# Kernel optimization log

Hardware: AMD Instinct MI355X
Metric: run time of the kernel (lower is better)

Reference implementation:

```python
import jax, jax.numpy as jnp
import numpy as np
import math

B, T, IN_DIM = 4, 1024, 64
D, H, L, DFF = 1024, 16, 4, 4096
N_STEPS = 24
MAXLEN = 2048
DK = D // H


def _pos_encoding(max_len, d):
    pos = np.arange(max_len, dtype=np.float32)[:, None]
    div = np.exp(np.arange(0, d, 2, dtype=np.float32) * (-math.log(10000.0) / d))
    pe = np.zeros((max_len, d), dtype=np.float32)
    pe[:, 0::2] = np.sin(pos * div)
    pe[:, 1::2] = np.cos(pos * div)
    return jnp.asarray(pe)

_PE = _pos_encoding(MAXLEN, D)


def _lin(x, W, b):
    # torch Linear convention: W is (out, in)
    return x @ W.T + b


def _mha(q, kv, Wq, bq, Wk, bk, Wv, bv, Wo, bo):
    Bq, Tq, _ = q.shape
    Tk = kv.shape[1]
    Qh = _lin(q, Wq, bq).reshape(Bq, Tq, H, DK).transpose(0, 2, 1, 3)
    Kh = _lin(kv, Wk, bk).reshape(Bq, Tk, H, DK).transpose(0, 2, 1, 3)
    Vh = _lin(kv, Wv, bv).reshape(Bq, Tk, H, DK).transpose(0, 2, 1, 3)
    scores = jnp.einsum('bhqd,bhkd->bhqk', Qh, Kh) / math.sqrt(DK)
    probs = jax.nn.softmax(scores, axis=-1)
    out = jnp.einsum('bhqk,bhkd->bhqd', probs, Vh)
    out = out.transpose(0, 2, 1, 3).reshape(Bq, Tq, D)
    return _lin(out, Wo, bo)


def _ffn(x, W1, b1, W2, b2):
    return _lin(jax.nn.relu(_lin(x, W1, b1)), W2, b2)


def _ln(x, g, b, eps=1e-5):
    mu = jnp.mean(x, axis=-1, keepdims=True)
    var = jnp.var(x, axis=-1, keepdims=True)
    return (x - mu) / jnp.sqrt(var + eps) * g + b


def setup_inputs() -> dict:
    key = jax.random.key(0)
    ks = iter(jax.random.split(key, 64))
    def w(shape, s=0.02):
        return jax.random.normal(next(ks), shape, jnp.float32) * s
    inp = {'x': jax.random.normal(next(ks), (B, T, IN_DIM), jnp.float32)}
    inp['in_W'] = w((D, IN_DIM)); inp['in_b'] = jnp.zeros((D,), jnp.float32)
    for p in ['enc', 'dec']:
        for n in ['Wq', 'Wk', 'Wv', 'Wo']:
            inp[f'{p}_{n}'] = w((L, D, D))
            inp[f'{p}_b{n[1].lower()}'] = jnp.zeros((L, D), jnp.float32)
    for p in ['ffe', 'ffd']:
        inp[f'{p}_W1'] = w((DFF, D)); inp[f'{p}_b1'] = jnp.zeros((DFF,), jnp.float32)
        inp[f'{p}_W2'] = w((D, DFF)); inp[f'{p}_b2'] = jnp.zeros((D,), jnp.float32)
    for p in ['ne', 'nd']:
        inp[f'{p}_g'] = jnp.ones((D,), jnp.float32); inp[f'{p}_b'] = jnp.zeros((D,), jnp.float32)
    inp['out_W'] = w((1, D)); inp['out_b'] = jnp.zeros((1,), jnp.float32)
    inp['temb_W'] = w((D, 1)); inp['temb_b'] = jnp.zeros((D,), jnp.float32)
    return inp


def reference(x, in_W, in_b,
              enc_Wq, enc_bq, enc_Wk, enc_bk, enc_Wv, enc_bv, enc_Wo, enc_bo,
              ffe_W1, ffe_b1, ffe_W2, ffe_b2, ne_g, ne_b,
              dec_Wq, dec_bq, dec_Wk, dec_bk, dec_Wv, dec_bv, dec_Wo, dec_bo,
              ffd_W1, ffd_b1, ffd_W2, ffd_b2, nd_g, nd_b,
              out_W, out_b, temb_W, temb_b):
    batch, seq, _ = x.shape
    h = _lin(x, in_W, in_b) + _PE[:seq]
    for l in range(L):
        h = _mha(h, h, enc_Wq[l], enc_bq[l], enc_Wk[l], enc_bk[l],
                 enc_Wv[l], enc_bv[l], enc_Wo[l], enc_bo[l])
        h = _ln(h + _ffn(h, ffe_W1, ffe_b1, ffe_W2, ffe_b2), ne_g, ne_b)
    dec = jnp.zeros((batch, 1, D), x.dtype)
    preds = []
    for _ in range(N_STEPS):
        d = dec + _PE[:dec.shape[1]]
        for l in range(L):
            # same layer weights used for self- and cross-attention, as in source
            d = _mha(d, d, dec_Wq[l], dec_bq[l], dec_Wk[l], dec_bk[l],
                     dec_Wv[l], dec_bv[l], dec_Wo[l], dec_bo[l])
            d = _mha(d, h, dec_Wq[l], dec_bq[l], dec_Wk[l], dec_bk[l],
                     dec_Wv[l], dec_bv[l], dec_Wo[l], dec_bo[l])
            d = _ln(d + _ffn(d, ffd_W1, ffd_b1, ffd_W2, ffd_b2), nd_g, nd_b)
        step = _lin(d[:, -1, :], out_W, out_b)        # (B, 1)
        preds.append(step[:, None, :])                 # (B, 1, 1)
        emb = _lin(step, temb_W, temb_b)[:, None, :]   # (B, 1, D)
        dec = jnp.concatenate([dec, emb], axis=1)
    return jnp.concatenate(preds, axis=1)              # (B, n_steps, 1)
```

## Files before the change

kernel.cpp:

```cpp
#include <hip/hip_runtime.h>
#include <math.h>

#define DM    1024
#define NH    16
#define DKH   64
#define NL    4
#define DFFN  4096
#define BB    4
#define TT    1024
#define NSTEP 24
#define BT    (BB*TT)
#define MD    (BB*NSTEP)
#define CSPLIT 8
#define CKEYS  (TT/CSPLIT)

typedef __attribute__((ext_vector_type(8))) short s16x8;
typedef __attribute__((ext_vector_type(4))) short s16x4;
typedef __attribute__((ext_vector_type(4))) float f32x4;

__device__ inline short f2b(float f){
  unsigned u = __float_as_uint(f);
  u += 0x7fffu + ((u>>16)&1u);
  return (short)(u>>16);
}
__device__ inline float b2f(short h){
  return __uint_as_float(((unsigned)(unsigned short)h)<<16);
}

__global__ __launch_bounds__(256)
void split_kernel(const float* __restrict__ X, short* __restrict__ Hi,
                  short* __restrict__ Lo, int n8)
{
  const size_t i = (size_t)blockIdx.x*256 + threadIdx.x;
  if (i >= (size_t)n8) return;
  const float4 v0 = *(const float4*)(X + i*8);
  const float4 v1 = *(const float4*)(X + i*8 + 4);
  const float f[8] = {v0.x,v0.y,v0.z,v0.w,v1.x,v1.y,v1.z,v1.w};
  s16x8 hv, lv;
  #pragma unroll
  for (int e=0;e<8;e++){
    const short h = f2b(f[e]);
    hv[e] = h;
    lv[e] = f2b(f[e] - b2f(h));
  }
  *(s16x8*)(Hi + i*8) = hv;
  *(s16x8*)(Lo + i*8) = lv;
}

__global__ void zero_kernel(float* __restrict__ p, int n) {
  int i = blockIdx.x*256 + threadIdx.x;
  if (i < n) p[i] = 0.f;
}

__global__ __launch_bounds__(256)
void add_pe_split(const float* __restrict__ h, short* __restrict__ Hi,
                  short* __restrict__ Lo)
{
  const int row = blockIdx.x;
  const int pos = row & (TT-1);
  const int d = threadIdx.x*4;
  const float4 a = *(const float4*)(h + (size_t)row*DM + d);
  const float c1 = -9.210340371976184f / 1024.0f;
  const float e0 = expf((float)d * c1);
  const float e1 = expf((float)(d+2) * c1);
  const float a0 = (float)pos * e0, a1 = (float)pos * e1;
  const float v[4] = {a.x + sinf(a0), a.y + cosf(a0), a.z + sinf(a1), a.w + cosf(a1)};
  s16x4 hv, lv;
  #pragma unroll
  for (int e=0;e<4;e++){
    const short hb = f2b(v[e]);
    hv[e] = hb;
    lv[e] = f2b(v[e] - b2f(hb));
  }
  *(s16x4*)(Hi + (size_t)row*DM + d) = hv;
  *(s16x4*)(Lo + (size_t)row*DM + d) = lv;
}

__global__ __launch_bounds__(256)
void dec_prep_split(short* __restrict__ Dhi, short* __restrict__ Dlo,
                    const float* __restrict__ tok)
{
  const int r = blockIdx.x;
  const int i = r >> 2;
  const int d = threadIdx.x*4;
  const float4 a = *(const float4*)(tok + (size_t)r*DM + d);
  const float c1 = -9.210340371976184f / 1024.0f;
  const float e0 = expf((float)d * c1);
  const float e1 = expf((float)(d+2) * c1);
  const float a0 = (float)i * e0, a1 = (float)i * e1;
  const float v[4] = {a.x + sinf(a0), a.y + cosf(a0), a.z + sinf(a1), a.w + cosf(a1)};
  s16x4 hv, lv;
  #pragma unroll
  for (int e=0;e<4;e++){
    const short hb = f2b(v[e]);
    hv[e] = hb;
    lv[e] = f2b(v[e] - b2f(hb));
  }
  *(s16x4*)(Dhi + (size_t)r*DM + d) = hv;
  *(s16x4*)(Dlo + (size_t)r*DM + d) = lv;
}

template<int ACT, int OUT_MODE>
__global__ __launch_bounds__(256, 2)
void gemm_split(const short* __restrict__ Ahi, const short* __restrict__ Alo,
                const short* __restrict__ Bhi, const short* __restrict__ Blo,
                const float* __restrict__ bias,
                float* __restrict__ C, short* __restrict__ Chi, short* __restrict__ Clo,
                int M, int N, int K)
{
  __shared__ __align__(16) short lA[2][128][40];
  __shared__ __align__(16) short lB[2][128][40];
  const int tid = threadIdx.x;
  const int m0 = blockIdx.x*128, n0 = blockIdx.y*128;
  const int lane = tid & 63, w = tid >> 6;
  const int wr = w >> 1, wc = w & 1;
  const int fr = lane & 15, fq = lane >> 4;

  f32x4 acc[4][4];
  #pragma unroll
  for (int i=0;i<4;i++)
    #pragma unroll
    for (int j=0;j<4;j++) acc[i][j] = (f32x4){0.f,0.f,0.f,0.f};

  for (int k0 = 0; k0 < K; k0 += 32) {
    __syncthreads();
    #pragma unroll
    for (int j=0;j<2;j++){
      const int cc = tid + j*256;
      const int row = cc >> 2, kq = cc & 3;
      const size_t ga = (size_t)(m0+row)*K + k0 + kq*8;
      const size_t gb = (size_t)(n0+row)*K + k0 + kq*8;
      *(s16x8*)&lA[0][row][kq*8] = *(const s16x8*)(Ahi + ga);
      *(s16x8*)&lA[1][row][kq*8] = *(const s16x8*)(Alo + ga);
      *(s16x8*)&lB[0][row][kq*8] = *(const s16x8*)(Bhi + gb);
      *(s16x8*)&lB[1][row][kq*8] = *(const s16x8*)(Blo + gb);
    }
    __syncthreads();
    s16x8 ah[4], al[4], bh[4], bl[4];
    #pragma unroll
    for (int i=0;i<4;i++){
      ah[i] = *(const s16x8*)&lA[0][wr*64+i*16+fr][fq*8];
      al[i] = *(const s16x8*)&lA[1][wr*64+i*16+fr][fq*8];
    }
    #pragma unroll
    for (int j=0;j<4;j++){
      bh[j] = *(const s16x8*)&lB[0][wc*64+j*16+fr][fq*8];
      bl[j] = *(const s16x8*)&lB[1][wc*64+j*16+fr][fq*8];
    }
    #pragma unroll
    for (int i=0;i<4;i++)
      #pragma unroll
      for (int j=0;j<4;j++){
        acc[i][j] = __builtin_amdgcn_mfma_f32_16x16x32_bf16(ah[i], bh[j], acc[i][j], 0,0,0);
        acc[i][j] = __builtin_amdgcn_mfma_f32_16x16x32_bf16(ah[i], bl[j], acc[i][j], 0,0,0);
        acc[i][j] = __builtin_amdgcn_mfma_f32_16x16x32_bf16(al[i], bh[j], acc[i][j], 0,0,0);
      }
  }
  #pragma unroll
  for (int j=0;j<4;j++){
    const int col = n0 + wc*64 + j*16 + fr;
    const float bv = bias[col];
    #pragma unroll
    for (int i=0;i<4;i++){
      const int row0 = m0 + wr*64 + i*16 + fq*4;
      #pragma unroll
      for (int r=0;r<4;r++){
        float v = acc[i][j][r] + bv;
        if (ACT==1) v = fmaxf(v, 0.f);
        const size_t idx = (size_t)(row0+r)*N + col;
        if (OUT_MODE==0 || OUT_MODE==2) C[idx] = v;
        if (OUT_MODE==1 || OUT_MODE==2){
          const short hb = f2b(v);
          Chi[idx] = hb;
          Clo[idx] = f2b(v - b2f(hb));
        }
        if (OUT_MODE==3) Chi[idx] = f2b(v);
      }
    }
  }
}

template<int MR>
__global__ __launch_bounds__(256)
void gemm_dec(const short* __restrict__ Ahi, const short* __restrict__ Alo,
              const short* __restrict__ B0hi, const short* __restrict__ B0lo,
              const short* __restrict__ B1hi, const short* __restrict__ B1lo,
              const short* __restrict__ B2hi, const short* __restrict__ B2lo,
              float* __restrict__ part, int N, int K, int KS)
{
  const short* Bhi = (blockIdx.z==0) ? B0hi : (blockIdx.z==1 ? B1hi : B2hi);
  const short* Blo = (blockIdx.z==0) ? B0lo : (blockIdx.z==1 ? B1lo : B2lo);
  float* P = part + ((size_t)blockIdx.z*KS + blockIdx.y)*(size_t)MD*N;
  const int KK = K / KS;
  const int kbase = blockIdx.y * KK;
  const int n0 = blockIdx.x * 128;
  __shared__ __align__(16) short lA[2][96][40];
  __shared__ __align__(16) short lB[2][128][40];
  const int tid = threadIdx.x;
  const int lane = tid & 63, w = tid >> 6;
  const int fr = lane & 15, fq = lane >> 4;
  constexpr int CH = MR*128;

  f32x4 acc[MR][2];
  #pragma unroll
  for (int i=0;i<MR;i++){ acc[i][0]=(f32x4){0,0,0,0}; acc[i][1]=(f32x4){0,0,0,0}; }

  for (int k0 = kbase; k0 < kbase + KK; k0 += 32) {
    __syncthreads();
    #pragma unroll
    for (int t=0; t<(CH+255)/256; t++){
      const int cc = tid + t*256;
      if (cc < CH){
        const int row = cc>>3, hl = (cc>>2)&1, kq = cc&3;
        const short* src = hl ? Alo : Ahi;
        *(s16x8*)&lA[hl][row][kq*8] = *(const s16x8*)(src + (size_t)row*K + k0 + kq*8);
      }
    }
    #pragma unroll
    for (int t=0; t<4; t++){
      const int cc = tid + t*256;
      const int row = cc>>3, hl = (cc>>2)&1, kq = cc&3;
      const short* src = hl ? Blo : Bhi;
      *(s16x8*)&lB[hl][row][kq*8] = *(const s16x8*)(src + (size_t)(n0+row)*K + k0 + kq*8);
    }
    __syncthreads();
    s16x8 bh[2], bl[2];
    #pragma unroll
    for (int j=0;j<2;j++){
      bh[j] = *(const s16x8*)&lB[0][w*32+j*16+fr][fq*8];
      bl[j] = *(const s16x8*)&lB[1][w*32+j*16+fr][fq*8];
    }
    #pragma unroll
    for (int i=0;i<MR;i++){
      const s16x8 ah = *(const s16x8*)&lA[0][i*16+fr][fq*8];
      const s16x8 al = *(const s16x8*)&lA[1][i*16+fr][fq*8];
      #pragma unroll
      for (int j=0;j<2;j++){
        acc[i][j] = __builtin_amdgcn_mfma_f32_16x16x32_bf16(ah, bh[j], acc[i][j], 0,0,0);
        acc[i][j] = __builtin_amdgcn_mfma_f32_16x16x32_bf16(ah, bl[j], acc[i][j], 0,0,0);
        acc[i][j] = __builtin_amdgcn_mfma_f32_16x16x32_bf16(al, bh[j], acc[i][j], 0,0,0);
      }
    }
  }
  #pragma unroll
  for (int j=0;j<2;j++){
    const int col = n0 + w*32 + j*16 + fr;
    #pragma unroll
    for (int i=0;i<MR;i++){
      const int row0 = i*16 + fq*4;
      #pragma unroll
      for (int r=0;r<4;r++)
        P[(size_t)(row0+r)*N + col] = acc[i][j][r];
    }
  }
}

template<int ACT, int MODE>
__global__ __launch_bounds__(256)
void reduce_dec(const float* __restrict__ part,
                const float* __restrict__ b0, const float* __restrict__ b1,
                const float* __restrict__ b2,
                float* __restrict__ o0, float* __restrict__ o1, float* __restrict__ o2,
                short* __restrict__ ohi, short* __restrict__ olo,
                int N, int KS)
{
  const int idx = blockIdx.x*256 + threadIdx.x;
  const int z = blockIdx.y;
  const float* P = part + (size_t)z*KS*(size_t)MD*N;
  const float* bias = (z==0)?b0:(z==1?b1:b2);
  float* out = (z==0)?o0:(z==1?o1:o2);
  float s = 0.f;
  for (int ks=0; ks<KS; ks++) s += P[(size_t)ks*MD*N + idx];
  s += bias[idx & (N-1)];
  if (ACT==1) s = fmaxf(s, 0.f);
  if (MODE==0 || MODE==2) out[idx] = s;
  if (MODE==1 || MODE==2){
    if (z==0){
      const short hb = f2b(s);
      ohi[idx] = hb;
      olo[idx] = f2b(s - b2f(hb));
    }
  }
}

__global__ __launch_bounds__(256)
void attn_enc(const float* __restrict__ Qg, const float* __restrict__ Kg,
              const float* __restrict__ Vg, short* __restrict__ Ohi,
              short* __restrict__ Olo)
{
  const int bh = blockIdx.y;
  const int b = bh >> 4, hh = bh & 15;
  const int row = blockIdx.x*256 + threadIdx.x;
  const size_t base = ((size_t)b*TT)*DM + hh*DKH;
  float q[64];
  {
    const float* qp = Qg + base + (size_t)row*DM;
    #pragma unroll
    for (int d4=0; d4<16; d4++){
      const float4 v = *(const float4*)(qp + d4*4);
      q[d4*4+0]=v.x; q[d4*4+1]=v.y; q[d4*4+2]=v.z; q[d4*4+3]=v.w;
    }
  }
  float o[64];
  #pragma unroll
  for (int d=0;d<64;d++) o[d]=0.f;
  float m = -INFINITY, l = 0.f;
  __shared__ float Ks[64][68];
  __shared__ float Vs[64][68];
  for (int kt=0; kt<TT; kt+=64) {
    __syncthreads();
    #pragma unroll
    for (int t=0;t<4;t++){
      const int fi = threadIdx.x + t*256;
      const int j = fi>>4, dq = fi&15;
      *(float4*)&Ks[j][dq*4] = *(const float4*)(Kg + base + (size_t)(kt+j)*DM + dq*4);
      *(float4*)&Vs[j][dq*4] = *(const float4*)(Vg + base + (size_t)(kt+j)*DM + dq*4);
    }
    __syncthreads();
    for (int j=0;j<64;j++){
      float s0=0.f,s1=0.f,s2=0.f,s3=0.f;
      #pragma unroll
      for (int d=0; d<64; d+=4){
        s0 = fmaf(q[d+0], Ks[j][d+0], s0);
        s1 = fmaf(q[d+1], Ks[j][d+1], s1);
        s2 = fmaf(q[d+2], Ks[j][d+2], s2);
        s3 = fmaf(q[d+3], Ks[j][d+3], s3);
      }
      const float s = ((s0+s1)+(s2+s3)) * 0.125f;
      if (s > m) {
        const float f = __expf(m - s);
        l *= f;
        #pragma unroll
        for (int d=0;d<64;d++) o[d] *= f;
        m = s;
      }
      const float p = __expf(s - m);
      l += p;
      #pragma unroll
      for (int d=0;d<64;d++) o[d] = fmaf(p, Vs[j][d], o[d]);
    }
  }
  const float inv = 1.f / l;
  #pragma unroll
  for (int d8=0; d8<8; d8++){
    s16x8 hv, lv;
    #pragma unroll
    for (int e=0;e<8;e++){
      const float f = o[d8*8+e]*inv;
      const short hb = f2b(f);
      hv[e] = hb;
      lv[e] = f2b(f - b2f(hb));
    }
    *(s16x8*)(Ohi + base + (size_t)row*DM + d8*8) = hv;
    *(s16x8*)(Olo + base + (size_t)row*DM + d8*8) = lv;
  }
}

__global__ __launch_bounds__(256)
void attn_dec_selfp(const float* __restrict__ Qg, const float* __restrict__ Kg,
                    const float* __restrict__ Vg, short* __restrict__ Ohi,
                    short* __restrict__ Olo, int n)
{
  const int b = blockIdx.x >> 4, hh = blockIdx.x & 15;
  const size_t base = (size_t)b*DM + hh*DKH;
  __shared__ float Qs[NSTEP][68], Ks[NSTEP][68], Vs[NSTEP][68];
  __shared__ float P[NSTEP][28];
  const int tid = threadIdx.x;
  for (int t = tid; t < 3*n*16; t += 256) {
    const int tensor = t / (n*16);
    const int fi = t - tensor*(n*16);
    const int row = fi >> 4, dq = fi & 15;
    const float* src = (tensor==0?Qg:(tensor==1?Kg:Vg)) + base + (size_t)(row*4)*DM + dq*4;
    float (*dst)[68] = (tensor==0?Qs:(tensor==1?Ks:Vs));
    *(float4*)&dst[row][dq*4] = *(const float4*)src;
  }
  __syncthreads();
  for (int idx = tid; idx < n*n; idx += 256) {
    const int i = idx / n, j = idx - i*n;
    float s0=0.f,s1=0.f,s2=0.f,s3=0.f;
    #pragma unroll
    for (int d=0; d<64; d+=4){
      s0 = fmaf(Qs[i][d+0], Ks[j][d+0], s0);
      s1 = fmaf(Qs[i][d+1], Ks[j][d+1], s1);
      s2 = fmaf(Qs[i][d+2], Ks[j][d+2], s2);
      s3 = fmaf(Qs[i][d+3], Ks[j][d+3], s3);
    }
    P[i][j] = ((s0+s1)+(s2+s3))*0.125f;
  }
  __syncthreads();
  if (tid < n) {
    float mm = -INFINITY;
    for (int j=0;j<n;j++) mm = fmaxf(mm, P[tid][j]);
    float l = 0.f;
    for (int j=0;j<n;j++){ const float p = __expf(P[tid][j]-mm); P[tid][j]=p; l+=p; }
    const float inv = 1.f/l;
    for (int j=0;j<n;j++) P[tid][j] *= inv;
  }
  __syncthreads();
  for (int idx = tid; idx < n*64; idx += 256){
    const int i = idx >> 6, d = idx & 63;
    float s = 0.f;
    for (int j=0;j<n;j++) s = fmaf(P[i][j], Vs[j][d], s);
    const short hb = f2b(s);
    const size_t o = base + (size_t)(i*4)*DM + d;
    Ohi[o] = hb;
    Olo[o] = f2b(s - b2f(hb));
  }
}

__global__ __launch_bounds__(256)
void attn_cross_part(const float* __restrict__ Qg, const short* __restrict__ Kc,
                     const short* __restrict__ Vc, float* __restrict__ opart,
                     float* __restrict__ mlpart, int n)
{
  const int ks = blockIdx.x;
  const int bh = blockIdx.y;
  const int b = bh >> 4, hh = bh & 15;
  __shared__ float Qs[NSTEP][68];
  __shared__ float KVs[CKEYS][68];
  __shared__ float S[NSTEP][CKEYS+4];
  const int tid = threadIdx.x;
  const size_t qbase = (size_t)b*DM + hh*DKH;
  for (int t=tid; t<n*16; t+=256){
    const int row = t>>4, dq = t&15;
    *(float4*)&Qs[row][dq*4] = *(const float4*)(Qg + qbase + (size_t)(row*4)*DM + dq*4);
  }
  const size_t kbase = ((size_t)b*TT + (size_t)ks*CKEYS)*DM + hh*DKH;
  for (int t=tid; t<CKEYS*8; t+=256){
    const int row = t>>3, d8 = t&7;
    const s16x8 v = *(const s16x8*)(Kc + kbase + (size_t)row*DM + d8*8);
    #pragma unroll
    for (int e=0;e<8;e++) KVs[row][d8*8+e] = b2f(v[e]);
  }
  __syncthreads();
  for (int idx=tid; idx<n*128; idx+=256){
    const int i = idx >> 7, j = idx & 127;
    float s0=0.f,s1=0.f,s2=0.f,s3=0.f;
    #pragma unroll
    for (int d=0; d<64; d+=4){
      s0 = fmaf(Qs[i][d+0], KVs[j][d+0], s0);
      s1 = fmaf(Qs[i][d+1], KVs[j][d+1], s1);
      s2 = fmaf(Qs[i][d+2], KVs[j][d+2], s2);
      s3 = fmaf(Qs[i][d+3], KVs[j][d+3], s3);
    }
    S[i][j] = ((s0+s1)+(s2+s3))*0.125f;
  }
  __syncthreads();
  for (int t=tid; t<CKEYS*8; t+=256){
    const int row = t>>3, d8 = t&7;
    const s16x8 v = *(const s16x8*)(Vc + kbase + (size_t)row*DM + d8*8);
    #pragma unroll
    for (int e=0;e<8;e++) KVs[row][d8*8+e] = b2f(v[e]);
  }
  if (tid < n){
    float mm=-INFINITY;
    for (int j=0;j<CKEYS;j++) mm = fmaxf(mm, S[tid][j]);
    float l=0.f;
    for (int j=0;j<CKEYS;j++){ const float p=__expf(S[tid][j]-mm); S[tid][j]=p; l+=p; }
    mlpart[((size_t)bh*CSPLIT+ks)*(2*NSTEP) + tid*2+0] = mm;
    mlpart[((size_t)bh*CSPLIT+ks)*(2*NSTEP) + tid*2+1] = l;
  }
  __syncthreads();
  for (int idx=tid; idx<n*64; idx+=256){
    const int i = idx >> 6, d = idx & 63;
    float s=0.f;
    for (int j=0;j<CKEYS;j++) s = fmaf(S[i][j], KVs[j][d], s);
    opart[(((size_t)bh*CSPLIT+ks)*NSTEP + i)*DKH + d] = s;
  }
}

__global__ __launch_bounds__(256)
void attn_cross_comb(const float* __restrict__ opart, const float* __restrict__ mlpart,
                     short* __restrict__ Ohi, short* __restrict__ Olo, int n)
{
  const int bh = blockIdx.x;
  const int idx = blockIdx.y*256 + threadIdx.x;
  const int i = idx >> 6, d = idx & 63;
  if (i >= n) return;
  float M = -INFINITY;
  #pragma unroll
  for (int s=0;s<CSPLIT;s++)
    M = fmaxf(M, mlpart[((size_t)bh*CSPLIT+s)*(2*NSTEP) + i*2]);
  float acc = 0.f, L = 0.f;
  #pragma unroll
  for (int s=0;s<CSPLIT;s++){
    const float mm = mlpart[((size_t)bh*CSPLIT+s)*(2*NSTEP) + i*2+0];
    const float ll = mlpart[((size_t)bh*CSPLIT+s)*(2*NSTEP) + i*2+1];
    const float f = __expf(mm - M);
    acc = fmaf(f, opart[(((size_t)bh*CSPLIT+s)*NSTEP + i)*DKH + d], acc);
    L   = fmaf(f, ll, L);
  }
  const int b = bh >> 4, hh = bh & 15;
  const float v = acc / L;
  const short hb = f2b(v);
  const size_t o = ((size_t)(i*4+b))*DM + hh*DKH + d;
  Ohi[o] = hb;
  Olo[o] = f2b(v - b2f(hb));
}

__device__ inline float wave_sum(float v){
  #pragma unroll
  for (int off=1; off<64; off<<=1) v += __shfl_xor(v, off, 64);
  return v;
}

__global__ __launch_bounds__(256)
void ln_add_split(const float* __restrict__ X, const float* __restrict__ Y,
                  const float* __restrict__ g, const float* __restrict__ be,
                  short* __restrict__ Ohi, short* __restrict__ Olo)
{
  const size_t row = blockIdx.x;
  const int tid = threadIdx.x;
  const float4 a = *(const float4*)(X + row*DM + tid*4);
  const float4 b = *(const float4*)(Y + row*DM + tid*4);
  const float v0=a.x+b.x, v1=a.y+b.y, v2=a.z+b.z, v3=a.w+b.w;
  float s = v0+v1+v2+v3;
  float q = v0*v0+v1*v1+v2*v2+v3*v3;
  s = wave_sum(s); q = wave_sum(q);
  __shared__ float rs[4], rq[4];
  if ((tid&63)==0){ rs[tid>>6]=s; rq[tid>>6]=q; }
  __syncthreads();
  const float S = rs[0]+rs[1]+rs[2]+rs[3];
  const float Q = rq[0]+rq[1]+rq[2]+rq[3];
  const float mean = S * (1.f/DM);
  const float var  = Q * (1.f/DM) - mean*mean;
  const float rstd = rsqrtf(var + 1e-5f);
  const float4 gv = *(const float4*)(g  + tid*4);
  const float4 bv = *(const float4*)(be + tid*4);
  const float v[4] = {(v0-mean)*rstd*gv.x + bv.x, (v1-mean)*rstd*gv.y + bv.y,
                      (v2-mean)*rstd*gv.z + bv.z, (v3-mean)*rstd*gv.w + bv.w};
  s16x4 hv, lv;
  #pragma unroll
  for (int e=0;e<4;e++){
    const short hb = f2b(v[e]);
    hv[e] = hb;
    lv[e] = f2b(v[e] - b2f(hb));
  }
  *(s16x4*)(Ohi + row*DM + tid*4) = hv;
  *(s16x4*)(Olo + row*DM + tid*4) = lv;
}

__global__ __launch_bounds__(256)
void ln_add_dec(const float* __restrict__ X, const float* __restrict__ Y,
                const float* __restrict__ g, const float* __restrict__ be,
                float* __restrict__ Outf, short* __restrict__ Ohi,
                short* __restrict__ Olo)
{
  const size_t row = blockIdx.x;
  const int tid = threadIdx.x;
  const float4 a = *(const float4*)(X + row*DM + tid*4);
  const float4 b = *(const float4*)(Y + row*DM + tid*4);
  const float v0=a.x+b.x, v1=a.y+b.y, v2=a.z+b.z, v3=a.w+b.w;
  float s = v0+v1+v2+v3;
  float q = v0*v0+v1*v1+v2*v2+v3*v3;
  s = wave_sum(s); q = wave_sum(q);
  __shared__ float rs[4], rq[4];
  if ((tid&63)==0){ rs[tid>>6]=s; rq[tid>>6]=q; }
  __syncthreads();
  const float S = rs[0]+rs[1]+rs[2]+rs[3];
  const float Q = rq[0]+rq[1]+rq[2]+rq[3];
  const float mean = S * (1.f/DM);
  const float var  = Q * (1.f/DM) - mean*mean;
  const float rstd = rsqrtf(var + 1e-5f);
  const float4 gv = *(const float4*)(g  + tid*4);
  const float4 bv = *(const float4*)(be + tid*4);
  const float v[4] = {(v0-mean)*rstd*gv.x + bv.x, (v1-mean)*rstd*gv.y + bv.y,
                      (v2-mean)*rstd*gv.z + bv.z, (v3-mean)*rstd*gv.w + bv.w};
  float4 of; of.x=v[0]; of.y=v[1]; of.z=v[2]; of.w=v[3];
  *(float4*)(Outf + row*DM + tid*4) = of;
  s16x4 hv, lv;
  #pragma unroll
  for (int e=0;e<4;e++){
    const short hb = f2b(v[e]);
    hv[e] = hb;
    lv[e] = f2b(v[e] - b2f(hb));
  }
  *(s16x4*)(Ohi + row*DM + tid*4) = hv;
  *(s16x4*)(Olo + row*DM + tid*4) = lv;
}

__global__ __launch_bounds__(256)
void out_step(const float* __restrict__ Dv, const float* __restrict__ outW,
              const float* __restrict__ outB, const float* __restrict__ tembW,
              const float* __restrict__ tembB, float* __restrict__ dout,
              float* __restrict__ tok, int s)
{
  const int b = blockIdx.x;
  const int tid = threadIdx.x;
  const float* drow = Dv + ((size_t)(s*4 + b))*DM;
  const float4 dv = *(const float4*)(drow + tid*4);
  const float4 wv = *(const float4*)(outW + tid*4);
  float part = dv.x*wv.x + dv.y*wv.y + dv.z*wv.z + dv.w*wv.w;
  part = wave_sum(part);
  __shared__ float red[4];
  __shared__ float stepv;
  if ((tid&63)==0) red[tid>>6] = part;
  __syncthreads();
  if (tid==0) stepv = red[0]+red[1]+red[2]+red[3] + outB[0];
  __syncthreads();
  const float sv = stepv;
  if (tid==0) dout[b*NSTEP + s] = sv;
  if (s+1 < NSTEP) {
    const int d = tid*4;
    const float4 tw = *(const float4*)(tembW + d);
    const float4 tb = *(const float4*)(tembB + d);
    float4 e;
    e.x = fmaf(sv, tw.x, tb.x); e.y = fmaf(sv, tw.y, tb.y);
    e.z = fmaf(sv, tw.z, tb.z); e.w = fmaf(sv, tw.w, tb.w);
    *(float4*)(tok + ((size_t)((s+1)*4 + b))*DM + d) = e;
  }
}

extern "C" void kernel_launch(void* const* d_in, const int* in_sizes, int n_in,
                              void* d_out, int out_size, void* d_ws, size_t ws_size,
                              hipStream_t stream)
{
  (void)in_sizes; (void)n_in; (void)out_size; (void)ws_size;
  const float* x      = (const float*)d_in[0];
  const float* in_W   = (const float*)d_in[1];
  const float* in_b   = (const float*)d_in[2];
  const float* enc_Wq = (const float*)d_in[3];
  const float* enc_bq = (const float*)d_in[4];
  const float* enc_Wk = (const float*)d_in[5];
  const float* enc_bk = (const float*)d_in[6];
  const float* enc_Wv = (const float*)d_in[7];
  const float* enc_bv = (const float*)d_in[8];
  const float* enc_Wo = (const float*)d_in[9];
  const float* enc_bo = (const float*)d_in[10];
  const float* dec_Wq = (const float*)d_in[11];
  const float* dec_bq = (const float*)d_in[12];
  const float* dec_Wk = (const float*)d_in[13];
  const float* dec_bk = (const float*)d_in[14];
  const float* dec_Wv = (const float*)d_in[15];
  const float* dec_bv = (const float*)d_in[16];
  const float* dec_Wo = (const float*)d_in[17];
  const float* dec_bo = (const float*)d_in[18];
  const float* ffe_W1 = (const float*)d_in[19];
  const float* ffe_b1 = (const float*)d_in[20];
  const float* ffe_W2 = (const float*)d_in[21];
  const float* ffe_b2 = (const float*)d_in[22];
  const float* ffd_W1 = (const float*)d_in[23];
  const float* ffd_b1 = (const float*)d_in[24];
  const float* ffd_W2 = (const float*)d_in[25];
  const float* ffd_b2 = (const float*)d_in[26];
  const float* ne_g   = (const float*)d_in[27];
  const float* ne_b   = (const float*)d_in[28];
  const float* nd_g   = (const float*)d_in[29];
  const float* nd_b   = (const float*)d_in[30];
  const float* out_W  = (const float*)d_in[31];
  const float* out_b  = (const float*)d_in[32];
  const float* temb_W = (const float*)d_in[33];
  const float* temb_b = (const float*)d_in[34];
  float* dout = (float*)d_out;

  float* ws = (float*)d_ws;
  size_t off = 0;
  auto alloc  = [&](size_t n){ n = (n+3)&~(size_t)3; float* p = ws + off; off += n; return p; };
  auto allocS = [&](size_t n){ size_t nf = ((n+1)/2 + 3)&~(size_t)3; short* p = (short*)(ws + off); off += nf; return p; };

  short* hshi = allocS((size_t)BT*DM);
  short* hslo = allocS((size_t)BT*DM);
  float* h    = alloc((size_t)BT*DM);
  float* hn   = h;
  float* t0   = alloc((size_t)BT*DM);
  float* t1   = alloc((size_t)BT*DM);
  float* t2   = alloc((size_t)BT*DM);
  short* t3hi = allocS((size_t)BT*DM);
  short* t3lo = allocS((size_t)BT*DM);
  short* hnhi = allocS((size_t)BT*DM);
  short* hnlo = allocS((size_t)BT*DM);
  float* t4   = alloc((size_t)BT*DM);
  float* part = t4;
  short* fmhi = (short*)t0;
  short* fmlo = fmhi + (size_t)BT*DFFN;
  short* kcb  = allocS((size_t)NL*BT*DM);
  short* vcb  = allocS((size_t)NL*BT*DM);
  short* xshi = allocS((size_t)BT*64);
  short* xslo = allocS((size_t)BT*64);
  short* iwhi = allocS((size_t)DM*64);
  short* iwlo = allocS((size_t)DM*64);
  short* w0hi = allocS((size_t)DM*DM); short* w0lo = allocS((size_t)DM*DM);
  short* w1hi = allocS((size_t)DM*DM); short* w1lo = allocS((size_t)DM*DM);
  short* w2hi = allocS((size_t)DM*DM); short* w2lo = allocS((size_t)DM*DM);
  short* w3hi = allocS((size_t)DM*DM); short* w3lo = allocS((size_t)DM*DM);
  short* wfhi = allocS((size_t)DFFN*DM); short* wflo = allocS((size_t)DFFN*DM);
  float* tok  = alloc((size_t)MD*DM);
  float* dbuf = alloc((size_t)MD*DM);
  float* dq   = alloc((size_t)MD*DM);
  float* dk   = alloc((size_t)MD*DM);
  float* dv_  = alloc((size_t)MD*DM);
  float* dffo = alloc((size_t)MD*DM);
  short* dbhi = allocS((size_t)MD*DM);  short* dblo = allocS((size_t)MD*DM);
  short* dahi = allocS((size_t)MD*DM);  short* dalo = allocS((size_t)MD*DM);
  short* dmhi = allocS((size_t)MD*DFFN);short* dmlo = allocS((size_t)MD*DFFN);
  float* opart= alloc((size_t)BB*NH*CSPLIT*NSTEP*DKH);
  float* mlp  = alloc((size_t)BB*NH*CSPLIT*2*NSTEP);

  const size_t MM = (size_t)DM*DM;
  short* dwq = (short*)t0;
  short* dwk = (short*)t1;
  short* dwv = (short*)t2;
  short* dwo = (short*)h;
  short* fw1h = t3hi; short* fw1l = t3lo;
  short* fw2h = hnhi; short* fw2l = hnlo;

  auto cvt = [&](const float* src, short* hi, short* lo, size_t n){
    split_kernel<<<(int)((n/8 + 255)/256), 256, 0, stream>>>(src, hi, lo, (int)(n/8));
  };

  cvt(x,    xshi, xslo, (size_t)BT*64);
  cvt(in_W, iwhi, iwlo, (size_t)DM*64);
  zero_kernel<<<(MD*DM+255)/256, 256, 0, stream>>>(tok, MD*DM);

  gemm_split<0,0><<<dim3(BT/128, DM/128), 256, 0, stream>>>(
      xshi, xslo, iwhi, iwlo, in_b, h, (short*)nullptr, (short*)nullptr, BT, DM, 64);
  add_pe_split<<<BT, 256, 0, stream>>>(h, hshi, hslo);

  for (int l=0; l<NL; ++l) {
    const size_t wo = (size_t)l*DM*DM, bo_ = (size_t)l*DM;
    cvt(enc_Wq+wo, w0hi, w0lo, MM);
    cvt(enc_Wk+wo, w1hi, w1lo, MM);
    cvt(enc_Wv+wo, w2hi, w2lo, MM);
    cvt(enc_Wo+wo, w3hi, w3lo, MM);
    gemm_split<0,0><<<dim3(32,8),256,0,stream>>>(hshi, hslo, w0hi, w0lo, enc_bq+bo_,
        t0, (short*)nullptr, (short*)nullptr, BT, DM, DM);
    gemm_split<0,0><<<dim3(32,8),256,0,stream>>>(hshi, hslo, w1hi, w1lo, enc_bk+bo_,
        t1, (short*)nullptr, (short*)nullptr, BT, DM, DM);
    gemm_split<0,0><<<dim3(32,8),256,0,stream>>>(hshi, hslo, w2hi, w2lo, enc_bv+bo_,
        t2, (short*)nullptr, (short*)nullptr, BT, DM, DM);
    attn_enc<<<dim3(TT/256, BB*NH),256,0,stream>>>(t0, t1, t2, t3hi, t3lo);
    gemm_split<0,2><<<dim3(32,8),256,0,stream>>>(t3hi, t3lo, w3hi, w3lo, enc_bo+bo_,
        hn, hnhi, hnlo, BT, DM, DM);
    cvt(ffe_W1, wfhi, wflo, (size_t)DFFN*DM);
    gemm_split<1,1><<<dim3(32,32),256,0,stream>>>(hnhi, hnlo, wfhi, wflo, ffe_b1,
        (float*)nullptr, fmhi, fmlo, BT, DFFN, DM);
    cvt(ffe_W2, wfhi, wflo, (size_t)DM*DFFN);
    gemm_split<0,0><<<dim3(32,8),256,0,stream>>>(fmhi, fmlo, wfhi, wflo, ffe_b2,
        t4, (short*)nullptr, (short*)nullptr, BT, DM, DFFN);
    ln_add_split<<<BT,256,0,stream>>>(hn, t4, ne_g, ne_b, hshi, hslo);
  }

  for (int l=0; l<NL; ++l) {
    const size_t wo = (size_t)l*DM*DM, bo_ = (size_t)l*DM;
    cvt(dec_Wk+wo, w0hi, w0lo, MM);
    cvt(dec_Wv+wo, w1hi, w1lo, MM);
    gemm_split<0,3><<<dim3(32,8),256,0,stream>>>(hshi, hslo, w0hi, w0lo, dec_bk+bo_,
        (float*)nullptr, kcb+(size_t)l*BT*DM, (short*)nullptr, BT, DM, DM);
    gemm_split<0,3><<<dim3(32,8),256,0,stream>>>(hshi, hslo, w1hi, w1lo, dec_bv+bo_,
        (float*)nullptr, vcb+(size_t)l*BT*DM, (short*)nullptr, BT, DM, DM);
  }

  for (int l=0; l<NL; ++l) {
    const size_t wo = (size_t)l*DM*DM;
    cvt(dec_Wq+wo, dwq + (size_t)l*2*MM, dwq + (size_t)l*2*MM + MM, MM);
    cvt(dec_Wk+wo, dwk + (size_t)l*2*MM, dwk + (size_t)l*2*MM + MM, MM);
    cvt(dec_Wv+wo, dwv + (size_t)l*2*MM, dwv + (size_t)l*2*MM + MM, MM);
    cvt(dec_Wo+wo, dwo + (size_t)l*2*MM, dwo + (size_t)l*2*MM + MM, MM);
  }
  cvt(ffd_W1, fw1h, fw1l, (size_t)DFFN*DM);
  cvt(ffd_W2, fw2h, fw2l, (size_t)DM*DFFN);

  #define GD(MRv, grid, ...) do { switch(MRv){ \
    case 1: gemm_dec<1><<<grid,256,0,stream>>>(__VA_ARGS__); break; \
    case 2: gemm_dec<2><<<grid,256,0,stream>>>(__VA_ARGS__); break; \
    case 3: gemm_dec<3><<<grid,256,0,stream>>>(__VA_ARGS__); break; \
    case 4: gemm_dec<4><<<grid,256,0,stream>>>(__VA_ARGS__); break; \
    case 5: gemm_dec<5><<<grid,256,0,stream>>>(__VA_ARGS__); break; \
    default: gemm_dec<6><<<grid,256,0,stream>>>(__VA_ARGS__); break; } } while(0)

  for (int s=0; s<NSTEP; ++s) {
    const int n = s+1;
    const int rows = 4*n;
    const int Mt = (rows + 15) & ~15;
    const int MR = Mt >> 4;
    dec_prep_split<<<rows,256,0,stream>>>(dbhi, dblo, tok);
    for (int l=0; l<NL; ++l) {
      const size_t bo_ = (size_t)l*DM;
      short* qh = dwq + (size_t)l*2*MM; short* ql = qh + MM;
      short* kh = dwk + (size_t)l*2*MM; short* kl = kh + MM;
      short* vh = dwv + (size_t)l*2*MM; short* vl = vh + MM;
      short* oh = dwo + (size_t)l*2*MM; short* ol = oh + MM;
      GD(MR, dim3(8,8,3), dbhi,dblo, qh,ql, kh,kl, vh,vl, part, DM, DM, 8);
      reduce_dec<0,0><<<dim3(Mt*4,3),256,0,stream>>>(part, dec_bq+bo_, dec_bk+bo_, dec_bv+bo_,
          dq, dk, dv_, (short*)nullptr, (short*)nullptr, DM, 8);
      attn_dec_selfp<<<BB*NH,256,0,stream>>>(dq, dk, dv_, dahi, dalo, n);
      GD(MR, dim3(8,8,1), dahi,dalo, oh,ol, oh,ol, oh,ol, part, DM, DM, 8);
      reduce_dec<0,1><<<dim3(Mt*4,1),256,0,stream>>>(part, dec_bo+bo_, dec_bo+bo_, dec_bo+bo_,
          (float*)nullptr,(float*)nullptr,(float*)nullptr, dbhi, dblo, DM, 8);
      GD(MR, dim3(8,8,1), dbhi,dblo, qh,ql, qh,ql, qh,ql, part, DM, DM, 8);
      reduce_dec<0,0><<<dim3(Mt*4,1),256,0,stream>>>(part, dec_bq+bo_, dec_bq+bo_, dec_bq+bo_,
          dq, dq, dq, (short*)nullptr, (short*)nullptr, DM, 8);
      attn_cross_part<<<dim3(CSPLIT, BB*NH),256,0,stream>>>(dq, kcb+(size_t)l*BT*DM,
          vcb+(size_t)l*BT*DM, opart, mlp, n);
      attn_cross_comb<<<dim3(BB*NH, 6),256,0,stream>>>(opart, mlp, dahi, dalo, n);
      GD(MR, dim3(8,8,1), dahi,dalo, oh,ol, oh,ol, oh,ol, part, DM, DM, 8);
      reduce_dec<0,2><<<dim3(Mt*4,1),256,0,stream>>>(part, dec_bo+bo_, dec_bo+bo_, dec_bo+bo_,
          dbuf, dbuf, dbuf, dbhi, dblo, DM, 8);
      GD(MR, dim3(32,8,1), dbhi,dblo, fw1h,fw1l, fw1h,fw1l, fw1h,fw1l, part, DFFN, DM, 8);
      reduce_dec<1,1><<<dim3(Mt*16,1),256,0,stream>>>(part, ffd_b1, ffd_b1, ffd_b1,
          (float*)nullptr,(float*)nullptr,(float*)nullptr, dmhi, dmlo, DFFN, 8);
      GD(MR, dim3(8,16,1), dmhi,dmlo, fw2h,fw2l, fw2h,fw2l, fw2h,fw2l, part, DM, DFFN, 16);
      reduce_dec<0,0><<<dim3(Mt*4,1),256,0,stream>>>(part, ffd_b2, ffd_b2, ffd_b2,
          dffo, dffo, dffo, (short*)nullptr, (short*)nullptr, DM, 16);
      ln_add_dec<<<rows,256,0,stream>>>(dbuf, dffo, nd_g, nd_b, dbuf, dbhi, dblo);
    }
    out_step<<<BB,256,0,stream>>>(dbuf, out_W, out_b, temb_W, temb_b, dout, tok, s);
  }
  #undef GD
}
```

Measured before the change: 16.50 ms.

## Fold decoder out-projection into next Q projection and fuse decoder reduce kernels

Measured after the change: 13.60 ms. 17.6% less time.

```diff
diff --git a/kernel.cpp b/kernel.cpp
--- a/kernel.cpp
+++ b/kernel.cpp
@@ -13,6 +13,7 @@
 #define MD    (BB*NSTEP)
 #define CSPLIT 8
 #define CKEYS  (TT/CSPLIT)
+#define PSTRIDE ((size_t)MD*DM)
 
 typedef __attribute__((ext_vector_type(8))) short s16x8;
 typedef __attribute__((ext_vector_type(4))) short s16x4;
@@ -25,6 +26,12 @@
 }
 __device__ inline float b2f(short h){
   return __uint_as_float(((unsigned)(unsigned short)h)<<16);
+}
+
+__device__ inline float wave_sum(float v){
+  #pragma unroll
+  for (int off=1; off<64; off<<=1) v += __shfl_xor(v, off, 64);
+  return v;
 }
 
 __global__ __launch_bounds__(256)
@@ -50,6 +57,38 @@
 __global__ void zero_kernel(float* __restrict__ p, int n) {
   int i = blockIdx.x*256 + threadIdx.x;
   if (i < n) p[i] = 0.f;
+}
+
+__global__ __launch_bounds__(256)
+void k_transpose(const float* __restrict__ A, float* __restrict__ At)
+{
+  __shared__ float tile[32][33];
+  const int bx = blockIdx.x & 31, by = blockIdx.x >> 5;
+  const int x0 = bx*32, y0 = by*32;
+  const int tid = threadIdx.x;
+  for (int i=tid; i<1024; i+=256){
+    const int r = i>>5, c = i&31;
+    tile[r][c] = A[(size_t)(y0+r)*DM + x0+c];
+  }
+  __syncthreads();
+  for (int i=tid; i<1024; i+=256){
+    const int r = i>>5, c = i&31;
+    At[(size_t)(x0+r)*DM + y0+c] = tile[c][r];
+  }
+}
+
+__global__ __launch_bounds__(256)
+void k_bc(const float* __restrict__ Wq, const float* __restrict__ bo,
+          const float* __restrict__ bq, float* __restrict__ bc)
+{
+  const int row = blockIdx.x, tid = threadIdx.x;
+  float s = 0.f;
+  for (int j=tid; j<DM; j+=256) s += Wq[(size_t)row*DM + j]*bo[j];
+  s = wave_sum(s);
+  __shared__ float r4[4];
+  if ((tid&63)==0) r4[tid>>6] = s;
+  __syncthreads();
+  if (tid==0) bc[row] = r4[0]+r4[1]+r4[2]+r4[3] + bq[row];
 }
 
 __global__ __launch_bounds__(256)
@@ -74,30 +113,6 @@
   }
   *(s16x4*)(Hi + (size_t)row*DM + d) = hv;
   *(s16x4*)(Lo + (size_t)row*DM + d) = lv;
-}
-
-__global__ __launch_bounds__(256)
-void dec_prep_split(short* __restrict__ Dhi, short* __restrict__ Dlo,
-                    const float* __restrict__ tok)
-{
-  const int r = blockIdx.x;
-  const int i = r >> 2;
-  const int d = threadIdx.x*4;
-  const float4 a = *(const float4*)(tok + (size_t)r*DM + d);
-  const float c1 = -9.210340371976184f / 1024.0f;
-  const float e0 = expf((float)d * c1);
-  const float e1 = expf((float)(d+2) * c1);
-  const float a0 = (float)i * e0, a1 = (float)i * e1;
-  const float v[4] = {a.x + sinf(a0), a.y + cosf(a0), a.z + sinf(a1), a.w + cosf(a1)};
-  s16x4 hv, lv;
-  #pragma unroll
-  for (int e=0;e<4;e++){
-    const short hb = f2b(v[e]);
-    hv[e] = hb;
-    lv[e] = f2b(v[e] - b2f(hb));
-  }
-  *(s16x4*)(Dhi + (size_t)r*DM + d) = hv;
-  *(s16x4*)(Dlo + (size_t)r*DM + d) = lv;
 }
 
 template<int ACT, int OUT_MODE>
@@ -176,109 +191,6 @@
         }
         if (OUT_MODE==3) Chi[idx] = f2b(v);
       }
-    }
-  }
-}
-
-template<int MR>
-__global__ __launch_bounds__(256)
-void gemm_dec(const short* __restrict__ Ahi, const short* __restrict__ Alo,
-              const short* __restrict__ B0hi, const short* __restrict__ B0lo,
-              const short* __restrict__ B1hi, const short* __restrict__ B1lo,
-              const short* __restrict__ B2hi, const short* __restrict__ B2lo,
-              float* __restrict__ part, int N, int K, int KS)
-{
-  const short* Bhi = (blockIdx.z==0) ? B0hi : (blockIdx.z==1 ? B1hi : B2hi);
-  const short* Blo = (blockIdx.z==0) ? B0lo : (blockIdx.z==1 ? B1lo : B2lo);
-  float* P = part + ((size_t)blockIdx.z*KS + blockIdx.y)*(size_t)MD*N;
-  const int KK = K / KS;
-  const int kbase = blockIdx.y * KK;
-  const int n0 = blockIdx.x * 128;
-  __shared__ __align__(16) short lA[2][96][40];
-  __shared__ __align__(16) short lB[2][128][40];
-  const int tid = threadIdx.x;
-  const int lane = tid & 63, w = tid >> 6;
-  const int fr = lane & 15, fq = lane >> 4;
-  constexpr int CH = MR*128;
-
-  f32x4 acc[MR][2];
-  #pragma unroll
-  for (int i=0;i<MR;i++){ acc[i][0]=(f32x4){0,0,0,0}; acc[i][1]=(f32x4){0,0,0,0}; }
-
-  for (int k0 = kbase; k0 < kbase + KK; k0 += 32) {
-    __syncthreads();
-    #pragma unroll
-    for (int t=0; t<(CH+255)/256; t++){
-      const int cc = tid + t*256;
-      if (cc < CH){
-        const int row = cc>>3, hl = (cc>>2)&1, kq = cc&3;
-        const short* src = hl ? Alo : Ahi;
-        *(s16x8*)&lA[hl][row][kq*8] = *(const s16x8*)(src + (size_t)row*K + k0 + kq*8);
-      }
-    }
-    #pragma unroll
-    for (int t=0; t<4; t++){
-      const int cc = tid + t*256;
-      const int row = cc>>3, hl = (cc>>2)&1, kq = cc&3;
-      const short* src = hl ? Blo : Bhi;
-      *(s16x8*)&lB[hl][row][kq*8] = *(const s16x8*)(src + (size_t)(n0+row)*K + k0 + kq*8);
-    }
-    __syncthreads();
-    s16x8 bh[2], bl[2];
-    #pragma unroll
-    for (int j=0;j<2;j++){
-      bh[j] = *(const s16x8*)&lB[0][w*32+j*16+fr][fq*8];
-      bl[j] = *(const s16x8*)&lB[1][w*32+j*16+fr][fq*8];
-    }
-    #pragma unroll
-    for (int i=0;i<MR;i++){
-      const s16x8 ah = *(const s16x8*)&lA[0][i*16+fr][fq*8];
-      const s16x8 al = *(const s16x8*)&lA[1][i*16+fr][fq*8];
-      #pragma unroll
-      for (int j=0;j<2;j++){
-        acc[i][j] = __builtin_amdgcn_mfma_f32_16x16x32_bf16(ah, bh[j], acc[i][j], 0,0,0);
-        acc[i][j] = __builtin_amdgcn_mfma_f32_16x16x32_bf16(ah, bl[j], acc[i][j], 0,0,0);
-        acc[i][j] = __builtin_amdgcn_mfma_f32_16x16x32_bf16(al, bh[j], acc[i][j], 0,0,0);
-      }
-    }
-  }
-  #pragma unroll
-  for (int j=0;j<2;j++){
-    const int col = n0 + w*32 + j*16 + fr;
-    #pragma unroll
-    for (int i=0;i<MR;i++){
-      const int row0 = i*16 + fq*4;
-      #pragma unroll
-      for (int r=0;r<4;r++)
-        P[(size_t)(row0+r)*N + col] = acc[i][j][r];
-    }
-  }
-}
-
-template<int ACT, int MODE>
-__global__ __launch_bounds__(256)
-void reduce_dec(const float* __restrict__ part,
-                const float* __restrict__ b0, const float* __restrict__ b1,
-                const float* __restrict__ b2,
-                float* __restrict__ o0, float* __restrict__ o1, float* __restrict__ o2,
-                short* __restrict__ ohi, short* __restrict__ olo,
-                int N, int KS)
-{
-  const int idx = blockIdx.x*256 + threadIdx.x;
-  const int z = blockIdx.y;
-  const float* P = part + (size_t)z*KS*(size_t)MD*N;
-  const float* bias = (z==0)?b0:(z==1?b1:b2);
-  float* out = (z==0)?o0:(z==1?o1:o2);
-  float s = 0.f;
-  for (int ks=0; ks<KS; ks++) s += P[(size_t)ks*MD*N + idx];
-  s += bias[idx & (N-1)];
-  if (ACT==1) s = fmaxf(s, 0.f);
-  if (MODE==0 || MODE==2) out[idx] = s;
-  if (MODE==1 || MODE==2){
-    if (z==0){
-      const short hb = f2b(s);
-      ohi[idx] = hb;
-      olo[idx] = f2b(s - b2f(hb));
     }
   }
 }
@@ -357,154 +269,6 @@
 }
 
 __global__ __launch_bounds__(256)
-void attn_dec_selfp(const float* __restrict__ Qg, const float* __restrict__ Kg,
-                    const float* __restrict__ Vg, short* __restrict__ Ohi,
-                    short* __restrict__ Olo, int n)
-{
-  const int b = blockIdx.x >> 4, hh = blockIdx.x & 15;
-  const size_t base = (size_t)b*DM + hh*DKH;
-  __shared__ float Qs[NSTEP][68], Ks[NSTEP][68], Vs[NSTEP][68];
-  __shared__ float P[NSTEP][28];
-  const int tid = threadIdx.x;
-  for (int t = tid; t < 3*n*16; t += 256) {
-    const int tensor = t / (n*16);
-    const int fi = t - tensor*(n*16);
-    const int row = fi >> 4, dq = fi & 15;
-    const float* src = (tensor==0?Qg:(tensor==1?Kg:Vg)) + base + (size_t)(row*4)*DM + dq*4;
-    float (*dst)[68] = (tensor==0?Qs:(tensor==1?Ks:Vs));
-    *(float4*)&dst[row][dq*4] = *(const float4*)src;
-  }
-  __syncthreads();
-  for (int idx = tid; idx < n*n; idx += 256) {
-    const int i = idx / n, j = idx - i*n;
-    float s0=0.f,s1=0.f,s2=0.f,s3=0.f;
-    #pragma unroll
-    for (int d=0; d<64; d+=4){
-      s0 = fmaf(Qs[i][d+0], Ks[j][d+0], s0);
-      s1 = fmaf(Qs[i][d+1], Ks[j][d+1], s1);
-      s2 = fmaf(Qs[i][d+2], Ks[j][d+2], s2);
-      s3 = fmaf(Qs[i][d+3], Ks[j][d+3], s3);
-    }
-    P[i][j] = ((s0+s1)+(s2+s3))*0.125f;
-  }
-  __syncthreads();
-  if (tid < n) {
-    float mm = -INFINITY;
-    for (int j=0;j<n;j++) mm = fmaxf(mm, P[tid][j]);
-    float l = 0.f;
-    for (int j=0;j<n;j++){ const float p = __expf(P[tid][j]-mm); P[tid][j]=p; l+=p; }
-    const float inv = 1.f/l;
-    for (int j=0;j<n;j++) P[tid][j] *= inv;
-  }
-  __syncthreads();
-  for (int idx = tid; idx < n*64; idx += 256){
-    const int i = idx >> 6, d = idx & 63;
-    float s = 0.f;
-    for (int j=0;j<n;j++) s = fmaf(P[i][j], Vs[j][d], s);
-    const short hb = f2b(s);
-    const size_t o = base + (size_t)(i*4)*DM + d;
-    Ohi[o] = hb;
-    Olo[o] = f2b(s - b2f(hb));
-  }
-}
-
-__global__ __launch_bounds__(256)
-void attn_cross_part(const float* __restrict__ Qg, const short* __restrict__ Kc,
-                     const short* __restrict__ Vc, float* __restrict__ opart,
-                     float* __restrict__ mlpart, int n)
-{
-  const int ks = blockIdx.x;
-  const int bh = blockIdx.y;
-  const int b = bh >> 4, hh = bh & 15;
-  __shared__ float Qs[NSTEP][68];
-  __shared__ float KVs[CKEYS][68];
-  __shared__ float S[NSTEP][CKEYS+4];
-  const int tid = threadIdx.x;
-  const size_t qbase = (size_t)b*DM + hh*DKH;
-  for (int t=tid; t<n*16; t+=256){
-    const int row = t>>4, dq = t&15;
-    *(float4*)&Qs[row][dq*4] = *(const float4*)(Qg + qbase + (size_t)(row*4)*DM + dq*4);
-  }
-  const size_t kbase = ((size_t)b*TT + (size_t)ks*CKEYS)*DM + hh*DKH;
-  for (int t=tid; t<CKEYS*8; t+=256){
-    const int row = t>>3, d8 = t&7;
-    const s16x8 v = *(const s16x8*)(Kc + kbase + (size_t)row*DM + d8*8);
-    #pragma unroll
-    for (int e=0;e<8;e++) KVs[row][d8*8+e] = b2f(v[e]);
-  }
-  __syncthreads();
-  for (int idx=tid; idx<n*128; idx+=256){
-    const int i = idx >> 7, j = idx & 127;
-    float s0=0.f,s1=0.f,s2=0.f,s3=0.f;
-    #pragma unroll
-    for (int d=0; d<64; d+=4){
-      s0 = fmaf(Qs[i][d+0], KVs[j][d+0], s0);
-      s1 = fmaf(Qs[i][d+1], KVs[j][d+1], s1);
-      s2 = fmaf(Qs[i][d+2], KVs[j][d+2], s2);
-      s3 = fmaf(Qs[i][d+3], KVs[j][d+3], s3);
-    }
-    S[i][j] = ((s0+s1)+(s2+s3))*0.125f;
-  }
-  __syncthreads();
-  for (int t=tid; t<CKEYS*8; t+=256){
-    const int row = t>>3, d8 = t&7;
-    const s16x8 v = *(const s16x8*)(Vc + kbase + (size_t)row*DM + d8*8);
-    #pragma unroll
-    for (int e=0;e<8;e++) KVs[row][d8*8+e] = b2f(v[e]);
-  }
-  if (tid < n){
-    float mm=-INFINITY;
-    for (int j=0;j<CKEYS;j++) mm = fmaxf(mm, S[tid][j]);
-    float l=0.f;
-    for (int j=0;j<CKEYS;j++){ const float p=__expf(S[tid][j]-mm); S[tid][j]=p; l+=p; }
-    mlpart[((size_t)bh*CSPLIT+ks)*(2*NSTEP) + tid*2+0] = mm;
-    mlpart[((size_t)bh*CSPLIT+ks)*(2*NSTEP) + tid*2+1] = l;
-  }
-  __syncthreads();
-  for (int idx=tid; idx<n*64; idx+=256){
-    const int i = idx >> 6, d = idx & 63;
-    float s=0.f;
-    for (int j=0;j<CKEYS;j++) s = fmaf(S[i][j], KVs[j][d], s);
-    opart[(((size_t)bh*CSPLIT+ks)*NSTEP + i)*DKH + d] = s;
-  }
-}
-
-__global__ __launch_bounds__(256)
-void attn_cross_comb(const float* __restrict__ opart, const float* __restrict__ mlpart,
-                     short* __restrict__ Ohi, short* __restrict__ Olo, int n)
-{
-  const int bh = blockIdx.x;
-  const int idx = blockIdx.y*256 + threadIdx.x;
-  const int i = idx >> 6, d = idx & 63;
-  if (i >= n) return;
-  float M = -INFINITY;
-  #pragma unroll
-  for (int s=0;s<CSPLIT;s++)
-    M = fmaxf(M, mlpart[((size_t)bh*CSPLIT+s)*(2*NSTEP) + i*2]);
-  float acc = 0.f, L = 0.f;
-  #pragma unroll
-  for (int s=0;s<CSPLIT;s++){
-    const float mm = mlpart[((size_t)bh*CSPLIT+s)*(2*NSTEP) + i*2+0];
-    const float ll = mlpart[((size_t)bh*CSPLIT+s)*(2*NSTEP) + i*2+1];
-    const float f = __expf(mm - M);
-    acc = fmaf(f, opart[(((size_t)bh*CSPLIT+s)*NSTEP + i)*DKH + d], acc);
-    L   = fmaf(f, ll, L);
-  }
-  const int b = bh >> 4, hh = bh & 15;
-  const float v = acc / L;
-  const short hb = f2b(v);
-  const size_t o = ((size_t)(i*4+b))*DM + hh*DKH + d;
-  Ohi[o] = hb;
-  Olo[o] = f2b(v - b2f(hb));
-}
-
-__device__ inline float wave_sum(float v){
-  #pragma unroll
-  for (int off=1; off<64; off<<=1) v += __shfl_xor(v, off, 64);
-  return v;
-}
-
-__global__ __launch_bounds__(256)
 void ln_add_split(const float* __restrict__ X, const float* __restrict__ Y,
                   const float* __restrict__ g, const float* __restrict__ be,
                   short* __restrict__ Ohi, short* __restrict__ Olo)
@@ -540,21 +304,278 @@
   *(s16x4*)(Olo + row*DM + tid*4) = lv;
 }
 
-__global__ __launch_bounds__(256)
-void ln_add_dec(const float* __restrict__ X, const float* __restrict__ Y,
-                const float* __restrict__ g, const float* __restrict__ be,
-                float* __restrict__ Outf, short* __restrict__ Ohi,
-                short* __restrict__ Olo)
-{
-  const size_t row = blockIdx.x;
+
+template<int MR>
+__global__ __launch_bounds__(256)
+void gemm_dec(const short* __restrict__ Ahi, const short* __restrict__ Alo,
+              const short* __restrict__ B0hi, const short* __restrict__ B0lo,
+              const short* __restrict__ B1hi, const short* __restrict__ B1lo,
+              const short* __restrict__ B2hi, const short* __restrict__ B2lo,
+              float* __restrict__ part, int N, int K, int KS)
+{
+  const short* Bhi = (blockIdx.z==0) ? B0hi : (blockIdx.z==1 ? B1hi : B2hi);
+  const short* Blo = (blockIdx.z==0) ? B0lo : (blockIdx.z==1 ? B1lo : B2lo);
+  float* P = part + ((size_t)blockIdx.z*KS + blockIdx.y)*(size_t)MD*N;
+  const int KK = K / KS;
+  const int kbase = blockIdx.y * KK;
+  const int n0 = blockIdx.x * 128;
+  __shared__ __align__(16) short lA[2][96][40];
+  __shared__ __align__(16) short lB[2][128][40];
   const int tid = threadIdx.x;
-  const float4 a = *(const float4*)(X + row*DM + tid*4);
-  const float4 b = *(const float4*)(Y + row*DM + tid*4);
-  const float v0=a.x+b.x, v1=a.y+b.y, v2=a.z+b.z, v3=a.w+b.w;
+  const int lane = tid & 63, w = tid >> 6;
+  const int fr = lane & 15, fq = lane >> 4;
+  constexpr int CH = MR*128;
+
+  f32x4 acc[MR][2];
+  #pragma unroll
+  for (int i=0;i<MR;i++){ acc[i][0]=(f32x4){0,0,0,0}; acc[i][1]=(f32x4){0,0,0,0}; }
+
+  for (int k0 = kbase; k0 < kbase + KK; k0 += 32) {
+    __syncthreads();
+    #pragma unroll
+    for (int t=0; t<(CH+255)/256; t++){
+      const int cc = tid + t*256;
+      if (cc < CH){
+        const int row = cc>>3, hl = (cc>>2)&1, kq = cc&3;
+        const short* src = hl ? Alo : Ahi;
+        *(s16x8*)&lA[hl][row][kq*8] = *(const s16x8*)(src + (size_t)row*K + k0 + kq*8);
+      }
+    }
+    #pragma unroll
+    for (int t=0; t<4; t++){
+      const int cc = tid + t*256;
+      const int row = cc>>3, hl = (cc>>2)&1, kq = cc&3;
+      const short* src = hl ? Blo : Bhi;
+      *(s16x8*)&lB[hl][row][kq*8] = *(const s16x8*)(src + (size_t)(n0+row)*K + k0 + kq*8);
+    }
+    __syncthreads();
+    s16x8 bh[2], bl[2];
+    #pragma unroll
+    for (int j=0;j<2;j++){
+      bh[j] = *(const s16x8*)&lB[0][w*32+j*16+fr][fq*8];
+      bl[j] = *(const s16x8*)&lB[1][w*32+j*16+fr][fq*8];
+    }
+    #pragma unroll
+    for (int i=0;i<MR;i++){
+      const s16x8 ah = *(const s16x8*)&lA[0][i*16+fr][fq*8];
+      const s16x8 al = *(const s16x8*)&lA[1][i*16+fr][fq*8];
+      #pragma unroll
+      for (int j=0;j<2;j++){
+        acc[i][j] = __builtin_amdgcn_mfma_f32_16x16x32_bf16(ah, bh[j], acc[i][j], 0,0,0);
+        acc[i][j] = __builtin_amdgcn_mfma_f32_16x16x32_bf16(ah, bl[j], acc[i][j], 0,0,0);
+        acc[i][j] = __builtin_amdgcn_mfma_f32_16x16x32_bf16(al, bh[j], acc[i][j], 0,0,0);
+      }
+    }
+  }
+  #pragma unroll
+  for (int j=0;j<2;j++){
+    const int col = n0 + w*32 + j*16 + fr;
+    #pragma unroll
+    for (int i=0;i<MR;i++){
+      const int row0 = i*16 + fq*4;
+      #pragma unroll
+      for (int r=0;r<4;r++)
+        P[(size_t)(row0+r)*N + col] = acc[i][j][r];
+    }
+  }
+}
+
+template<int ACT, int MODE>
+__global__ __launch_bounds__(256)
+void reduce_dec(const float* __restrict__ part,
+                const float* __restrict__ b0, const float* __restrict__ b1,
+                const float* __restrict__ b2,
+                float* __restrict__ o0, float* __restrict__ o1, float* __restrict__ o2,
+                short* __restrict__ ohi, short* __restrict__ olo,
+                int N, int KS)
+{
+  const int idx = blockIdx.x*256 + threadIdx.x;
+  const int z = blockIdx.y;
+  const float* P = part + (size_t)z*KS*(size_t)MD*N;
+  const float* bias = (z==0)?b0:(z==1?b1:b2);
+  float* out = (z==0)?o0:(z==1?o1:o2);
+  float s = 0.f;
+  for (int ks=0; ks<KS; ks++) s += P[(size_t)ks*MD*N + idx];
+  s += bias[idx & (N-1)];
+  if (ACT==1) s = fmaxf(s, 0.f);
+  if (MODE==0 || MODE==2) out[idx] = s;
+  if (MODE==1 || MODE==2){
+    if (z==0){
+      const short hb = f2b(s);
+      ohi[idx] = hb;
+      olo[idx] = f2b(s - b2f(hb));
+    }
+  }
+}
+
+__global__ __launch_bounds__(256)
+void attn_qkv(const float* __restrict__ part,
+              const float* __restrict__ lbq, const float* __restrict__ lbk,
+              const float* __restrict__ lbv,
+              short* __restrict__ Ohi, short* __restrict__ Olo, int n)
+{
+  const int bh = blockIdx.x, b = bh >> 4, hh = bh & 15;
+  const size_t obase = (size_t)b*DM + hh*DKH;
+  __shared__ float Qs[NSTEP][68], Ks[NSTEP][68], Vs[NSTEP][68];
+  __shared__ float P[NSTEP][28];
+  const int tid = threadIdx.x;
+  for (int t = tid; t < 3*n*16; t += 256){
+    const int tensor = t / (n*16);
+    const int fi = t - tensor*(n*16);
+    const int row = fi >> 4, q4 = fi & 15;
+    const int col0 = hh*DKH + q4*4;
+    const float* bias = (tensor==0?lbq:(tensor==1?lbk:lbv));
+    float4 a;
+    a.x = bias[col0]; a.y = bias[col0+1]; a.z = bias[col0+2]; a.w = bias[col0+3];
+    const size_t eoff = (size_t)(row*4+b)*DM + col0;
+    #pragma unroll
+    for (int ks=0; ks<8; ks++){
+      const float4 p = *(const float4*)(part + (size_t)(tensor*8+ks)*PSTRIDE + eoff);
+      a.x+=p.x; a.y+=p.y; a.z+=p.z; a.w+=p.w;
+    }
+    float (*dst)[68] = (tensor==0?Qs:(tensor==1?Ks:Vs));
+    *(float4*)&dst[row][q4*4] = a;
+  }
+  __syncthreads();
+  for (int idx = tid; idx < n*n; idx += 256){
+    const int i = idx / n, j = idx - i*n;
+    float s0=0.f,s1=0.f,s2=0.f,s3=0.f;
+    #pragma unroll
+    for (int d=0; d<64; d+=4){
+      s0 = fmaf(Qs[i][d+0], Ks[j][d+0], s0);
+      s1 = fmaf(Qs[i][d+1], Ks[j][d+1], s1);
+      s2 = fmaf(Qs[i][d+2], Ks[j][d+2], s2);
+      s3 = fmaf(Qs[i][d+3], Ks[j][d+3], s3);
+    }
+    P[i][j] = ((s0+s1)+(s2+s3))*0.125f;
+  }
+  __syncthreads();
+  if (tid < n){
+    float mm = -INFINITY;
+    for (int j=0;j<n;j++) mm = fmaxf(mm, P[tid][j]);
+    float l = 0.f;
+    for (int j=0;j<n;j++){ const float p = __expf(P[tid][j]-mm); P[tid][j]=p; l+=p; }
+    const float inv = 1.f/l;
+    for (int j=0;j<n;j++) P[tid][j] *= inv;
+  }
+  __syncthreads();
+  for (int idx = tid; idx < n*64; idx += 256){
+    const int i = idx >> 6, d = idx & 63;
+    float s = 0.f;
+    for (int j=0;j<n;j++) s = fmaf(P[i][j], Vs[j][d], s);
+    const short hb = f2b(s);
+    const size_t o = obase + (size_t)(i*4)*DM + d;
+    Ohi[o] = hb;
+    Olo[o] = f2b(s - b2f(hb));
+  }
+}
+
+__global__ __launch_bounds__(256)
+void attn_cross_part(const float* __restrict__ Qg, const short* __restrict__ Kc,
+                     const short* __restrict__ Vc, float* __restrict__ opart,
+                     float* __restrict__ mlpart, int n)
+{
+  const int ks = blockIdx.x, bh = blockIdx.y;
+  const int b = bh >> 4, hh = bh & 15;
+  __shared__ float Qs[NSTEP][68];
+  __shared__ short KVs[CKEYS][72];
+  __shared__ float S[NSTEP][132];
+  const int tid = threadIdx.x;
+  const size_t qbase = (size_t)b*DM + hh*DKH;
+  for (int t=tid; t<n*16; t+=256){
+    const int row = t>>4, q4 = t&15;
+    *(float4*)&Qs[row][q4*4] = *(const float4*)(Qg + qbase + (size_t)(row*4)*DM + q4*4);
+  }
+  const size_t kbase = ((size_t)b*TT + (size_t)ks*CKEYS)*DM + hh*DKH;
+  for (int t=tid; t<CKEYS*8; t+=256){
+    const int row = t>>3, d8 = t&7;
+    *(s16x8*)&KVs[row][d8*8] = *(const s16x8*)(Kc + kbase + (size_t)row*DM + d8*8);
+  }
+  __syncthreads();
+  for (int idx=tid; idx<n*128; idx+=256){
+    const int i = idx >> 7, j = idx & 127;
+    float s0=0.f,s1=0.f,s2=0.f,s3=0.f;
+    #pragma unroll
+    for (int d=0; d<64; d+=4){
+      s0 = fmaf(Qs[i][d+0], b2f(KVs[j][d+0]), s0);
+      s1 = fmaf(Qs[i][d+1], b2f(KVs[j][d+1]), s1);
+      s2 = fmaf(Qs[i][d+2], b2f(KVs[j][d+2]), s2);
+      s3 = fmaf(Qs[i][d+3], b2f(KVs[j][d+3]), s3);
+    }
+    S[i][j] = ((s0+s1)+(s2+s3))*0.125f;
+  }
+  __syncthreads();
+  for (int t=tid; t<CKEYS*8; t+=256){
+    const int row = t>>3, d8 = t&7;
+    *(s16x8*)&KVs[row][d8*8] = *(const s16x8*)(Vc + kbase + (size_t)row*DM + d8*8);
+  }
+  if (tid < n){
+    float mm=-INFINITY;
+    for (int j=0;j<CKEYS;j++) mm = fmaxf(mm, S[tid][j]);
+    float l=0.f;
+    for (int j=0;j<CKEYS;j++){ const float p=__expf(S[tid][j]-mm); S[tid][j]=p; l+=p; }
+    mlpart[((size_t)bh*CSPLIT+ks)*(2*NSTEP) + tid*2+0] = mm;
+    mlpart[((size_t)bh*CSPLIT+ks)*(2*NSTEP) + tid*2+1] = l;
+  }
+  __syncthreads();
+  for (int idx=tid; idx<n*64; idx+=256){
+    const int i = idx >> 6, d = idx & 63;
+    float s=0.f;
+    for (int j=0;j<CKEYS;j++) s = fmaf(S[i][j], b2f(KVs[j][d]), s);
+    opart[(((size_t)bh*CSPLIT+ks)*NSTEP + i)*DKH + d] = s;
+  }
+}
+
+__global__ __launch_bounds__(256)
+void attn_cross_comb(const float* __restrict__ opart, const float* __restrict__ mlpart,
+                     short* __restrict__ Ohi, short* __restrict__ Olo, int n)
+{
+  const int bh = blockIdx.x;
+  const int idx = blockIdx.y*256 + threadIdx.x;
+  const int i = idx >> 6, d = idx & 63;
+  if (i >= n) return;
+  float M = -INFINITY;
+  #pragma unroll
+  for (int s=0;s<CSPLIT;s++)
+    M = fmaxf(M, mlpart[((size_t)bh*CSPLIT+s)*(2*NSTEP) + i*2]);
+  float acc = 0.f, L = 0.f;
+  #pragma unroll
+  for (int s=0;s<CSPLIT;s++){
+    const float mm = mlpart[((size_t)bh*CSPLIT+s)*(2*NSTEP) + i*2+0];
+    const float ll = mlpart[((size_t)bh*CSPLIT+s)*(2*NSTEP) + i*2+1];
+    const float f = __expf(mm - M);
+    acc = fmaf(f, opart[(((size_t)bh*CSPLIT+s)*NSTEP + i)*DKH + d], acc);
+    L   = fmaf(f, ll, L);
+  }
+  const int b = bh >> 4, hh = bh & 15;
+  const float v = acc / L;
+  const short hb = f2b(v);
+  const size_t o = ((size_t)(i*4+b))*DM + hh*DKH + d;
+  Ohi[o] = hb;
+  Olo[o] = f2b(v - b2f(hb));
+}
+
+__global__ __launch_bounds__(256)
+void k_lnr(const float* __restrict__ part, const float* __restrict__ bias,
+           const float* __restrict__ X, const float* __restrict__ g,
+           const float* __restrict__ be,
+           float* __restrict__ Outf, short* __restrict__ Ohi, short* __restrict__ Olo)
+{
+  const int row = blockIdx.x;
+  __shared__ float rs[4], rq[4];
+  const int tid = threadIdx.x;
+  float a0=0.f,a1=0.f,a2=0.f,a3=0.f;
+  #pragma unroll
+  for (int ks=0; ks<16; ks++){
+    const float4 p = *(const float4*)(part + (size_t)ks*PSTRIDE + (size_t)row*DM + tid*4);
+    a0+=p.x; a1+=p.y; a2+=p.z; a3+=p.w;
+  }
+  const float4 bvv = *(const float4*)(bias + tid*4);
+  const float4 xv  = *(const float4*)(X + (size_t)row*DM + tid*4);
+  const float v0=a0+bvv.x+xv.x, v1=a1+bvv.y+xv.y, v2=a2+bvv.z+xv.z, v3=a3+bvv.w+xv.w;
   float s = v0+v1+v2+v3;
   float q = v0*v0+v1*v1+v2*v2+v3*v3;
   s = wave_sum(s); q = wave_sum(q);
-  __shared__ float rs[4], rq[4];
   if ((tid&63)==0){ rs[tid>>6]=s; rq[tid>>6]=q; }
   __syncthreads();
   const float S = rs[0]+rs[1]+rs[2]+rs[3];
@@ -563,11 +584,11 @@
   const float var  = Q * (1.f/DM) - mean*mean;
   const float rstd = rsqrtf(var + 1e-5f);
   const float4 gv = *(const float4*)(g  + tid*4);
-  const float4 bv = *(const float4*)(be + tid*4);
-  const float v[4] = {(v0-mean)*rstd*gv.x + bv.x, (v1-mean)*rstd*gv.y + bv.y,
-                      (v2-mean)*rstd*gv.z + bv.z, (v3-mean)*rstd*gv.w + bv.w};
+  const float4 bv2 = *(const float4*)(be + tid*4);
+  const float v[4] = {(v0-mean)*rstd*gv.x + bv2.x, (v1-mean)*rstd*gv.y + bv2.y,
+                      (v2-mean)*rstd*gv.z + bv2.z, (v3-mean)*rstd*gv.w + bv2.w};
   float4 of; of.x=v[0]; of.y=v[1]; of.z=v[2]; of.w=v[3];
-  *(float4*)(Outf + row*DM + tid*4) = of;
+  *(float4*)(Outf + (size_t)row*DM + tid*4) = of;
   s16x4 hv, lv;
   #pragma unroll
   for (int e=0;e<4;e++){
@@ -575,40 +596,74 @@
     hv[e] = hb;
     lv[e] = f2b(v[e] - b2f(hb));
   }
-  *(s16x4*)(Ohi + row*DM + tid*4) = hv;
-  *(s16x4*)(Olo + row*DM + tid*4) = lv;
-}
-
-__global__ __launch_bounds__(256)
-void out_step(const float* __restrict__ Dv, const float* __restrict__ outW,
-              const float* __restrict__ outB, const float* __restrict__ tembW,
-              const float* __restrict__ tembB, float* __restrict__ dout,
-              float* __restrict__ tok, int s)
+  *(s16x4*)(Ohi + (size_t)row*DM + tid*4) = hv;
+  *(s16x4*)(Olo + (size_t)row*DM + tid*4) = lv;
+}
+
+__global__ __launch_bounds__(256)
+void k_out(const float* __restrict__ Dv, const float* __restrict__ outW,
+           const float* __restrict__ outB, const float* __restrict__ tembW,
+           const float* __restrict__ tembB, float* __restrict__ dout,
+           short* __restrict__ Dphi, short* __restrict__ Dplo, int s)
 {
   const int b = blockIdx.x;
+  __shared__ float red[4];
+  __shared__ float stepv;
   const int tid = threadIdx.x;
   const float* drow = Dv + ((size_t)(s*4 + b))*DM;
-  const float4 dv = *(const float4*)(drow + tid*4);
+  const float4 dv4 = *(const float4*)(drow + tid*4);
   const float4 wv = *(const float4*)(outW + tid*4);
-  float part = dv.x*wv.x + dv.y*wv.y + dv.z*wv.z + dv.w*wv.w;
-  part = wave_sum(part);
-  __shared__ float red[4];
-  __shared__ float stepv;
-  if ((tid&63)==0) red[tid>>6] = part;
-  __syncthreads();
-  if (tid==0) stepv = red[0]+red[1]+red[2]+red[3] + outB[0];
+  float p = dv4.x*wv.x + dv4.y*wv.y + dv4.z*wv.z + dv4.w*wv.w;
+  p = wave_sum(p);
+  if ((tid&63)==0) red[tid>>6] = p;
+  __syncthreads();
+  if (tid==0){
+    const float sv = red[0]+red[1]+red[2]+red[3] + outB[0];
+    stepv = sv;
+    dout[b*NSTEP + s] = sv;
+  }
   __syncthreads();
   const float sv = stepv;
-  if (tid==0) dout[b*NSTEP + s] = sv;
-  if (s+1 < NSTEP) {
-    const int d = tid*4;
+  if (s+1 < NSTEP){
+    const int d = tid*4, pos = s+1;
     const float4 tw = *(const float4*)(tembW + d);
     const float4 tb = *(const float4*)(tembB + d);
-    float4 e;
-    e.x = fmaf(sv, tw.x, tb.x); e.y = fmaf(sv, tw.y, tb.y);
-    e.z = fmaf(sv, tw.z, tb.z); e.w = fmaf(sv, tw.w, tb.w);
-    *(float4*)(tok + ((size_t)((s+1)*4 + b))*DM + d) = e;
-  }
+    const float c1 = -9.210340371976184f / 1024.0f;
+    const float e0 = expf((float)d * c1);
+    const float e1 = expf((float)(d+2) * c1);
+    const float a0 = (float)pos * e0, a1 = (float)pos * e1;
+    const float v[4] = { fmaf(sv, tw.x, tb.x) + sinf(a0),
+                         fmaf(sv, tw.y, tb.y) + cosf(a0),
+                         fmaf(sv, tw.z, tb.z) + sinf(a1),
+                         fmaf(sv, tw.w, tb.w) + cosf(a1) };
+    s16x4 hv, lv;
+    #pragma unroll
+    for (int e=0;e<4;e++){
+      const short hb = f2b(v[e]);
+      hv[e] = hb;
+      lv[e] = f2b(v[e] - b2f(hb));
+    }
+    const size_t o = (size_t)(pos*4 + b)*DM + d;
+    *(s16x4*)(Dphi + o) = hv;
+    *(s16x4*)(Dplo + o) = lv;
+  }
+}
+
+__global__ __launch_bounds__(256)
+void k_init0(short* __restrict__ Dphi, short* __restrict__ Dplo)
+{
+  const int b = blockIdx.x;
+  const int d = threadIdx.x*4;
+  const float v[4] = {0.f, 1.f, 0.f, 1.f};
+  s16x4 hv, lv;
+  #pragma unroll
+  for (int e=0;e<4;e++){
+    const short hb = f2b(v[e]);
+    hv[e] = hb;
+    lv[e] = f2b(v[e] - b2f(hb));
+  }
+  *(s16x4*)(Dphi + (size_t)b*DM + d) = hv;
+  *(s16x4*)(Dplo + (size_t)b*DM + d) = lv;
 }
 
 extern "C" void kernel_launch(void* const* d_in, const int* in_sizes, int n_in,
@@ -684,13 +739,14 @@
   short* w2hi = allocS((size_t)DM*DM); short* w2lo = allocS((size_t)DM*DM);
   short* w3hi = allocS((size_t)DM*DM); short* w3lo = allocS((size_t)DM*DM);
   short* wfhi = allocS((size_t)DFFN*DM); short* wflo = allocS((size_t)DFFN*DM);
-  float* tok  = alloc((size_t)MD*DM);
+  short* wf2hi= allocS((size_t)DM*DFFN); short* wf2lo= allocS((size_t)DM*DFFN);
+  float* bqo  = alloc((size_t)NL*DM);
+  float* zbuf = alloc((size_t)DM);
+  float* dq   = alloc((size_t)MD*DM);
   float* dbuf = alloc((size_t)MD*DM);
-  float* dq   = alloc((size_t)MD*DM);
-  float* dk   = alloc((size_t)MD*DM);
-  float* dv_  = alloc((size_t)MD*DM);
-  float* dffo = alloc((size_t)MD*DM);
-  short* dbhi = allocS((size_t)MD*DM);  short* dblo = allocS((size_t)MD*DM);
+  short* dphi = allocS((size_t)MD*DM);  short* dplo = allocS((size_t)MD*DM);
+  short* dlhi = allocS((size_t)MD*DM);  short* dllo = allocS((size_t)MD*DM);
+  short* dxhi = allocS((size_t)MD*DM);  short* dxlo = allocS((size_t)MD*DM);
   short* dahi = allocS((size_t)MD*DM);  short* dalo = allocS((size_t)MD*DM);
   short* dmhi = allocS((size_t)MD*DFFN);short* dmlo = allocS((size_t)MD*DFFN);
   float* opart= alloc((size_t)BB*NH*CSPLIT*NSTEP*DKH);
@@ -703,6 +759,9 @@
   short* dwo = (short*)h;
   short* fw1h = t3hi; short* fw1l = t3lo;
   short* fw2h = hnhi; short* fw2l = hnlo;
+  short* wch  = hshi; short* wcl  = hslo;
+  float* wotf = t4;
+  float* wcf  = t4 + MM;
 
   auto cvt = [&](const float* src, short* hi, short* lo, size_t n){
     split_kernel<<<(int)((n/8 + 255)/256), 256, 0, stream>>>(src, hi, lo, (int)(n/8));
@@ -710,7 +769,9 @@
 
   cvt(x,    xshi, xslo, (size_t)BT*64);
   cvt(in_W, iwhi, iwlo, (size_t)DM*64);
-  zero_kernel<<<(MD*DM+255)/256, 256, 0, stream>>>(tok, MD*DM);
+  cvt(ffe_W1, wfhi,  wflo,  (size_t)DFFN*DM);
+  cvt(ffe_W2, wf2hi, wf2lo, (size_t)DM*DFFN);
+  zero_kernel<<<(DM+255)/256, 256, 0, stream>>>(zbuf, DM);
 
   gemm_split<0,0><<<dim3(BT/128, DM/128), 256, 0, stream>>>(
       xshi, xslo, iwhi, iwlo, in_b, h, (short*)nullptr, (short*)nullptr, BT, DM, 64);
@@ -731,11 +792,9 @@
     attn_enc<<<dim3(TT/256, BB*NH),256,0,stream>>>(t0, t1, t2, t3hi, t3lo);
     gemm_split<0,2><<<dim3(32,8),256,0,stream>>>(t3hi, t3lo, w3hi, w3lo, enc_bo+bo_,
         hn, hnhi, hnlo, BT, DM, DM);
-    cvt(ffe_W1, wfhi, wflo, (size_t)DFFN*DM);
     gemm_split<1,1><<<dim3(32,32),256,0,stream>>>(hnhi, hnlo, wfhi, wflo, ffe_b1,
         (float*)nullptr, fmhi, fmlo, BT, DFFN, DM);
-    cvt(ffe_W2, wfhi, wflo, (size_t)DM*DFFN);
-    gemm_split<0,0><<<dim3(32,8),256,0,stream>>>(fmhi, fmlo, wfhi, wflo, ffe_b2,
+    gemm_split<0,0><<<dim3(32,8),256,0,stream>>>(fmhi, fmlo, wf2hi, wf2lo, ffe_b2,
         t4, (short*)nullptr, (short*)nullptr, BT, DM, DFFN);
     ln_add_split<<<BT,256,0,stream>>>(hn, t4, ne_g, ne_b, hshi, hslo);
   }
@@ -759,6 +818,16 @@
   }
   cvt(ffd_W1, fw1h, fw1l, (size_t)DFFN*DM);
   cvt(ffd_W2, fw2h, fw2l, (size_t)DM*DFFN);
+  for (int l=0; l<NL; ++l) {
+    const size_t wo = (size_t)l*DM*DM, bo_ = (size_t)l*DM;
+    k_transpose<<<1024, 256, 0, stream>>>(dec_Wo+wo, wotf);
+    cvt(wotf,      w0hi, w0lo, MM);
+    cvt(dec_Wq+wo, w1hi, w1lo, MM);
+    gemm_split<0,0><<<dim3(8,8),256,0,stream>>>(w1hi, w1lo, w0hi, w0lo, zbuf,
+        wcf, (short*)nullptr, (short*)nullptr, DM, DM, DM);
+    k_bc<<<DM, 256, 0, stream>>>(dec_Wq+wo, dec_bo+bo_, dec_bq+bo_, bqo+bo_);
+    cvt(wcf, wch + (size_t)l*MM, wcl + (size_t)l*MM, MM);
+  }
 
   #define GD(MRv, grid, ...) do { switch(MRv){ \
     case 1: gemm_dec<1><<<grid,256,0,stream>>>(__VA_ARGS__); break; \
@@ -768,43 +837,43 @@
     case 5: gemm_dec<5><<<grid,256,0,stream>>>(__VA_ARGS__); break; \
     default: gemm_dec<6><<<grid,256,0,stream>>>(__VA_ARGS__); break; } } while(0)
 
-  for (int s=0; s<NSTEP; ++s) {
-    const int n = s+1;
-    const int rows = 4*n;
+  k_init0<<<BB, 256, 0, stream>>>(dphi, dplo);
+  for (int s=0; s<NSTEP; ++s){
+    const int n = s+1, rows = 4*n;
     const int Mt = (rows + 15) & ~15;
     const int MR = Mt >> 4;
-    dec_prep_split<<<rows,256,0,stream>>>(dbhi, dblo, tok);
-    for (int l=0; l<NL; ++l) {
-      const size_t bo_ = (size_t)l*DM;
-      short* qh = dwq + (size_t)l*2*MM; short* ql = qh + MM;
-      short* kh = dwk + (size_t)l*2*MM; short* kl = kh + MM;
-      short* vh = dwv + (size_t)l*2*MM; short* vl = vh + MM;
-      short* oh = dwo + (size_t)l*2*MM; short* ol = oh + MM;
-      GD(MR, dim3(8,8,3), dbhi,dblo, qh,ql, kh,kl, vh,vl, part, DM, DM, 8);
-      reduce_dec<0,0><<<dim3(Mt*4,3),256,0,stream>>>(part, dec_bq+bo_, dec_bk+bo_, dec_bv+bo_,
-          dq, dk, dv_, (short*)nullptr, (short*)nullptr, DM, 8);
-      attn_dec_selfp<<<BB*NH,256,0,stream>>>(dq, dk, dv_, dahi, dalo, n);
-      GD(MR, dim3(8,8,1), dahi,dalo, oh,ol, oh,ol, oh,ol, part, DM, DM, 8);
-      reduce_dec<0,1><<<dim3(Mt*4,1),256,0,stream>>>(part, dec_bo+bo_, dec_bo+bo_, dec_bo+bo_,
-          (float*)nullptr,(float*)nullptr,(float*)nullptr, dbhi, dblo, DM, 8);
-      GD(MR, dim3(8,8,1), dbhi,dblo, qh,ql, qh,ql, qh,ql, part, DM, DM, 8);
-      reduce_dec<0,0><<<dim3(Mt*4,1),256,0,stream>>>(part, dec_bq+bo_, dec_bq+bo_, dec_bq+bo_,
+    for (int l=0; l<NL; ++l){
+      const short* qh = dwq + (size_t)l*2*MM; const short* ql = qh + MM;
+      const short* kh = dwk + (size_t)l*2*MM; const short* kl = kh + MM;
+      const short* vh = dwv + (size_t)l*2*MM; const short* vl = vh + MM;
+      const short* oh = dwo + (size_t)l*2*MM; const short* ol = oh + MM;
+      const short* ch = wch + (size_t)l*MM;   const short* cl = wcl + (size_t)l*MM;
+      const float* lbq = dec_bq + (size_t)l*DM;
+      const float* lbk = dec_bk + (size_t)l*DM;
+      const float* lbv = dec_bv + (size_t)l*DM;
+      const float* lbo = dec_bo + (size_t)l*DM;
+      const float* lbc = bqo + (size_t)l*DM;
+      const short* in_hi = (l==0) ? dphi : dlhi;
+      const short* in_lo = (l==0) ? dplo : dllo;
+      GD(MR, dim3(8,8,3), in_hi,in_lo, qh,ql, kh,kl, vh,vl, part, DM, DM, 8);
+      attn_qkv<<<BB*NH,256,0,stream>>>(part, lbq, lbk, lbv, dahi, dalo, n);
+      GD(MR, dim3(8,8,1), dahi,dalo, ch,cl, ch,cl, ch,cl, part, DM, DM, 8);
+      reduce_dec<0,0><<<dim3(Mt*4,1),256,0,stream>>>(part, lbc, lbc, lbc,
           dq, dq, dq, (short*)nullptr, (short*)nullptr, DM, 8);
-      attn_cross_part<<<dim3(CSPLIT, BB*NH),256,0,stream>>>(dq, kcb+(size_t)l*BT*DM,
-          vcb+(size_t)l*BT*DM, opart, mlp, n);
+      attn_cross_part<<<dim3(CSPLIT, BB*NH),256,0,stream>>>(dq,
+          kcb + (size_t)l*BT*DM, vcb + (size_t)l*BT*DM, opart, mlp, n);
       attn_cross_comb<<<dim3(BB*NH, 6),256,0,stream>>>(opart, mlp, dahi, dalo, n);
       GD(MR, dim3(8,8,1), dahi,dalo, oh,ol, oh,ol, oh,ol, part, DM, DM, 8);
-      reduce_dec<0,2><<<dim3(Mt*4,1),256,0,stream>>>(part, dec_bo+bo_, dec_bo+bo_, dec_bo+bo_,
-          dbuf, dbuf, dbuf, dbhi, dblo, DM, 8);
-      GD(MR, dim3(32,8,1), dbhi,dblo, fw1h,fw1l, fw1h,fw1l, fw1h,fw1l, part, DFFN, DM, 8);
+      reduce_dec<0,2><<<dim3(Mt*4,1),256,0,stream>>>(part, lbo, lbo, lbo,
+          dbuf, dbuf, dbuf, dxhi, dxlo, DM, 8);
+      GD(MR, dim3(32,8,1), dxhi,dxlo, fw1h,fw1l, fw1h,fw1l, fw1h,fw1l, part, DFFN, DM, 8);
       reduce_dec<1,1><<<dim3(Mt*16,1),256,0,stream>>>(part, ffd_b1, ffd_b1, ffd_b1,
           (float*)nullptr,(float*)nullptr,(float*)nullptr, dmhi, dmlo, DFFN, 8);
       GD(MR, dim3(8,16,1), dmhi,dmlo, fw2h,fw2l, fw2h,fw2l, fw2h,fw2l, part, DM, DFFN, 16);
-      reduce_dec<0,0><<<dim3(Mt*4,1),256,0,stream>>>(part, ffd_b2, ffd_b2, ffd_b2,
-          dffo, dffo, dffo, (short*)nullptr, (short*)nullptr, DM, 16);
-      ln_add_dec<<<rows,256,0,stream>>>(dbuf, dffo, nd_g, nd_b, dbuf, dbhi, dblo);
-    }
-    out_step<<<BB,256,0,stream>>>(dbuf, out_W, out_b, temb_W, temb_b, dout, tok, s);
+      k_lnr<<<rows,256,0,stream>>>(part, ffd_b2, dbuf, nd_g, nd_b, dbuf, dlhi, dllo);
+    }
+    k_out<<<BB, 256, 0, stream>>>(dbuf, out_W, out_b, temb_W, temb_b, dout,
+        dphi, dplo, s);
   }
   #undef GD
 }
```
